# Kernel tuning notes

Measured on AMD Instinct MI355X. Metric: run time of the kernel, lower is better.

The kernel has to match this reference:

```python
import jax, jax.numpy as jnp
import numpy as np

NOOBJ_LAMBDA = 0.5
COORD_LAMBDA = 5.0


def _cxcywh_to_xyxy(b):
    cx, cy, w, h = b[..., 0], b[..., 1], b[..., 2], b[..., 3]
    return jnp.stack([cx - w / 2, cy - h / 2, cx + w / 2, cy + h / 2], axis=-1)


def _pairwise_iou(a, b):
    # a: [B, N, 4] xyxy (preds), b: [B, M, 4] xyxy (targets) -> [B, N, M]
    lt = jnp.maximum(a[:, :, None, :2], b[:, None, :, :2])
    rb = jnp.minimum(a[:, :, None, 2:], b[:, None, :, 2:])
    wh = jnp.clip(rb - lt, 0.0)
    inter = wh[..., 0] * wh[..., 1]
    area_a = (a[..., 2] - a[..., 0]) * (a[..., 3] - a[..., 1])
    area_b = (b[..., 2] - b[..., 0]) * (b[..., 3] - b[..., 1])
    union = area_a[:, :, None] + area_b[:, None, :] - inter
    return inter / jnp.where(union > 0, union, 1.0)


def setup_inputs() -> dict:
    key = jax.random.key(0)
    kp, kt, km = jax.random.split(key, 3)
    B = 8192
    # positive values so sqrt(w), sqrt(h) is well-defined (as the torch code assumes)
    pred = jax.random.uniform(kp, (B, 7, 7, 30), dtype=jnp.float32, minval=0.05, maxval=1.0)
    target = jax.random.uniform(kt, (B, 7, 7, 30), dtype=jnp.float32, minval=0.05, maxval=1.0)
    # target confidence channel (index 4) is the obj/noobj indicator: 0 or 1
    obj = (jax.random.uniform(km, (B, 7, 7)) < 0.2).astype(jnp.float32)
    target = target.at[..., 4].set(obj)
    return {"pred_tensor": pred, "target_tensor": target}


def reference(pred_tensor, target_tensor):
    B = pred_tensor.shape[0]
    pred = pred_tensor.reshape(B, 49, 30)
    target = target_tensor.reshape(B, 49, 30)

    conf_t = target[..., 4]            # [B,49]
    noobj = conf_t == 0                # [B,49]
    obj = conf_t > 0                   # [B,49]

    # --- no-object confidence loss (channels 4 and 9) ---
    d4 = pred[..., 4] - target[..., 4]
    d9 = pred[..., 9] - target[..., 9]
    noobj_loss = jnp.sum(jnp.where(noobj, d4 * d4 + d9 * d9, 0.0))

    # --- object cells: 2 boxes per cell, padded to all 49 cells with a mask ---
    pb = pred[..., :10].reshape(B, 98, 5)
    tb = target[..., :10].reshape(B, 98, 5)
    box_mask = jnp.repeat(obj, 2, axis=1)  # [B,98]

    p_xyxy = _cxcywh_to_xyxy(pb[..., :4])
    t_xyxy = _cxcywh_to_xyxy(tb[..., :4])
    iou = _pairwise_iou(p_xyxy, t_xyxy)  # [B,98,98]
    pair_mask = box_mask[:, :, None] & box_mask[:, None, :]
    iou = jnp.where(pair_mask, iou, 0.0)
    max_iou = jnp.max(iou, axis=1)       # max over pred boxes, per target box [B,98]
    cmask = (max_iou != 0) & box_mask    # [B,98]

    cm = cmask.astype(pred.dtype)
    # coord (cx,cy) loss
    dxy = pb[..., :2] - tb[..., :2]
    coord_loss_cxcy = jnp.sum(cm * jnp.sum(dxy * dxy, axis=-1))
    # coord (sqrt w, sqrt h) loss
    dwh = jnp.sqrt(pb[..., 2:4]) - jnp.sqrt(tb[..., 2:4])
    coord_loss_wh = jnp.sum(cm * jnp.sum(dwh * dwh, axis=-1))
    # object confidence loss
    dconf = pb[..., 4] - tb[..., 4]
    obj_loss = jnp.sum(cm * dconf * dconf)

    # --- class loss over object cells ---
    dcls = pred[..., 10:] - target[..., 10:]
    cls_loss = jnp.sum(obj.astype(pred.dtype) * jnp.sum(dcls * dcls, axis=-1))

    bsz = jnp.asarray(B, pred.dtype)
    batch_cls_loss = cls_loss / bsz
    batch_obj_loss = (obj_loss + noobj_loss * NOOBJ_LAMBDA) / bsz
    batch_coord_loss = (coord_loss_cxcy + coord_loss_wh) * COORD_LAMBDA / bsz
    batch_loss = batch_cls_loss + batch_obj_loss + batch_coord_loss
    return (batch_loss, batch_cls_loss, batch_obj_loss, batch_coord_loss)
```

## Files before the change

kernel.cpp:

```cpp
#include <hip/hip_runtime.h>

#define CH 30
#define CELLS 49
#define ROWF 1470
#define RPW 2
#define WPB 4
#define RPB 8
#define NPAIR 735
#define NQ4 735
#define ITS 12

__device__ __forceinline__ float waveReduce(float v) {
    #pragma unroll
    for (int o = 32; o > 0; o >>= 1) v += __shfl_xor(v, o, 64);
    return v;
}

__global__ __launch_bounds__(256) void yolo_main(const float* __restrict__ pred,
                                                 const float* __restrict__ targ,
                                                 float* __restrict__ ws, int B,
                                                 int NB) {
    const int w = threadIdx.x >> 6;
    const int lane = threadIdx.x & 63;
    const int r0 = (blockIdx.x * WPB + w) * RPW;

    __shared__ float4 boxS[WPB][2 * CELLS];
    __shared__ int clist[WPB][CELLS];
    __shared__ float sred[WPB][3];

    float cls = 0.f, objc = 0.f, coord = 0.f;

    if (r0 < B) {
        const int nrows = (B - r0) >= RPW ? RPW : 1;
        const float* P = pred + (size_t)r0 * ROWF;
        const float* T = targ + (size_t)r0 * ROWF;
        unsigned long long m[2] = {0ull, 0ull};

        if (nrows == 2) {
            const float4* P4 = (const float4*)P;
            const float4* T4 = (const float4*)T;

            const int cl = lane < CELLS ? lane : CELLS - 1;
            const float conf0 = T[cl * CH + 4];
            const float conf1 = T[ROWF + cl * CH + 4];

            float4 pv[ITS], tv[ITS];
            #pragma unroll
            for (int it = 0; it < ITS; ++it) {
                const int j = lane + it * 64;
                const int jc = j < NQ4 ? j : NQ4 - 1;
                pv[it] = P4[jc];
                tv[it] = T4[jc];
            }

            const bool o0 = (lane < CELLS) && (conf0 > 0.f);
            const bool o1 = (lane < CELLS) && (conf1 > 0.f);
            m[0] = __ballot(o0);
            m[1] = __ballot(o1);

            #pragma unroll
            for (int it = 0; it < ITS; ++it) {
                const int j = lane + it * 64;
                const bool valid = j < NQ4;
                #pragma unroll
                for (int k = 0; k < 2; ++k) {
                    const int q = 2 * j + k;
                    const int row = q >= NPAIR ? 1 : 0;
                    const int pr = q - row * NPAIR;
                    const int cell = (pr * 17477) >> 18;
                    const int ch0 = 2 * (pr - cell * 15);
                    const float wobj = (float)((m[row] >> cell) & 1ull);
                    const float px = k ? pv[it].z : pv[it].x;
                    const float py = k ? pv[it].w : pv[it].y;
                    const float tx = k ? tv[it].z : tv[it].x;
                    const float ty = k ? tv[it].w : tv[it].y;
                    const float dx = px - tx, dy = py - ty;
                    cls += (valid && ch0 >= 10) ? wobj * (dx * dx + dy * dy) : 0.f;
                    const float nn = (ch0 == 4 ? dx * dx : 0.f)
                                   + (ch0 == 8 ? dy * dy : 0.f);
                    objc += valid ? 0.5f * (1.f - wobj) * nn : 0.f;
                }
            }
        } else {
            const float2* P2 = (const float2*)P;
            const float2* T2 = (const float2*)T;
            const int cl = lane < CELLS ? lane : CELLS - 1;
            const float conf = T[cl * CH + 4];
            const bool isObj = (lane < CELLS) && (conf > 0.f);
            m[0] = __ballot(isObj);
            for (int j = lane; j < NPAIR; j += 64) {
                const float2 pq = P2[j], tq = T2[j];
                const int cell = (j * 17477) >> 18;
                const int ch0 = 2 * (j - cell * 15);
                const float wobj = (float)((m[0] >> cell) & 1ull);
                const float dx = pq.x - tq.x, dy = pq.y - tq.y;
                cls += (ch0 >= 10) ? wobj * (dx * dx + dy * dy) : 0.f;
                const float nn = (ch0 == 4 ? dx * dx : 0.f)
                               + (ch0 == 8 ? dy * dy : 0.f);
                objc += 0.5f * (1.f - wobj) * nn;
            }
        }

        for (int rr = 0; rr < nrows; ++rr) {
            const unsigned long long mask = m[rr];
            const int nBox = 2 * __popcll(mask);
            if (nBox == 0) continue;
            const float* Pr = P + rr * ROWF;
            const float* Tr = T + rr * ROWF;

            const bool isObj = (lane < CELLS) && ((mask >> lane) & 1ull);
            if (isObj) clist[w][__popcll(mask & ((1ull << lane) - 1ull))] = lane;

            for (int e = lane; e < nBox; e += 64) {
                const int c = clist[w][e >> 1];
                const float* pb = Pr + c * CH + (e & 1) * 5;
                const float cx = pb[0], cy = pb[1], bw = pb[2], bh = pb[3];
                boxS[w][e] = make_float4(cx - 0.5f * bw, cy - 0.5f * bh,
                                         cx + 0.5f * bw, cy + 0.5f * bh);
            }

            for (int e = lane; e < nBox; e += 64) {
                const int c = clist[w][e >> 1];
                const float* tb = Tr + c * CH + (e & 1) * 5;
                const float tcx = tb[0], tcy = tb[1], tw = tb[2], th = tb[3];
                const float tx1 = tcx - 0.5f * tw, ty1 = tcy - 0.5f * th;
                const float tx2 = tcx + 0.5f * tw, ty2 = tcy + 0.5f * th;
                const float ta = (tx2 - tx1) * (ty2 - ty1);
                float maxiou = 0.f;
                for (int i = 0; i < nBox; ++i) {
                    const float4 pb4 = boxS[w][i];
                    const float lx = fmaxf(pb4.x, tx1), ly = fmaxf(pb4.y, ty1);
                    const float rx = fminf(pb4.z, tx2), ry = fminf(pb4.w, ty2);
                    const float iw = fmaxf(rx - lx, 0.f), ih = fmaxf(ry - ly, 0.f);
                    const float inter = iw * ih;
                    const float pa = (pb4.z - pb4.x) * (pb4.w - pb4.y);
                    const float un = pa + ta - inter;
                    const float iou = inter / (un > 0.f ? un : 1.f);
                    maxiou = fmaxf(maxiou, iou);
                }
                if (maxiou != 0.f) {
                    const float* pb = Pr + c * CH + (e & 1) * 5;
                    const float dcx = pb[0] - tcx, dcy = pb[1] - tcy;
                    coord += dcx * dcx + dcy * dcy;
                    const float dw = sqrtf(pb[2]) - sqrtf(tw);
                    const float dh = sqrtf(pb[3]) - sqrtf(th);
                    coord += dw * dw + dh * dh;
                    const float dc = pb[4] - tb[4];
                    objc += dc * dc;
                }
            }
        }
    }

    cls = waveReduce(cls); objc = waveReduce(objc); coord = waveReduce(coord);
    if (lane == 0) { sred[w][0] = cls; sred[w][1] = objc; sred[w][2] = coord; }
    __syncthreads();
    if (threadIdx.x == 0) {
        float C = 0.f, O = 0.f, X = 0.f;
        #pragma unroll
        for (int k = 0; k < WPB; ++k) { C += sred[k][0]; O += sred[k][1]; X += sred[k][2]; }
        ws[blockIdx.x] = C;
        ws[NB + blockIdx.x] = O;
        ws[2 * NB + blockIdx.x] = X;
    }
}

__global__ __launch_bounds__(1024) void yolo_reduce(const float* __restrict__ ws,
                                                    float* __restrict__ out,
                                                    int NB, float invB) {
    const int tid = threadIdx.x;
    const int w = tid >> 6, lane = tid & 63;
    float c = 0.f, o = 0.f, x = 0.f;
    for (int i = tid; i < NB; i += 1024) {
        c += ws[i];
        o += ws[NB + i];
        x += ws[2 * NB + i];
    }
    c = waveReduce(c); o = waveReduce(o); x = waveReduce(x);
    __shared__ float sred[16][3];
    if (lane == 0) { sred[w][0] = c; sred[w][1] = o; sred[w][2] = x; }
    __syncthreads();
    if (tid == 0) {
        float C = 0.f, O = 0.f, X = 0.f;
        #pragma unroll
        for (int k = 0; k < 16; ++k) { C += sred[k][0]; O += sred[k][1]; X += sred[k][2]; }
        const float bcls = C * invB;
        const float bobj = O * invB;
        const float bcoord = X * 5.0f * invB;
        out[0] = bcls + bobj + bcoord;
        out[1] = bcls;
        out[2] = bobj;
        out[3] = bcoord;
    }
}

extern "C" void kernel_launch(void* const* d_in, const int* in_sizes, int n_in,
                              void* d_out, int out_size, void* d_ws, size_t ws_size,
                              hipStream_t stream) {
    const float* pred = (const float*)d_in[0];
    const float* targ = (const float*)d_in[1];
    float* ws = (float*)d_ws;
    float* out = (float*)d_out;
    const int B = in_sizes[0] / ROWF;
    const int NB = (B + RPB - 1) / RPB;

    yolo_main<<<NB, 256, 0, stream>>>(pred, targ, ws, B, NB);
    yolo_reduce<<<1, 1024, 0, stream>>>(ws, out, NB, 1.0f / (float)B);
}
```

Baseline: 125.7 us.

## Split each row pair across two waves with software-pipelined loads and occupancy hint

```diff
diff --git a/kernel.cpp b/kernel.cpp
--- a/kernel.cpp
+++ b/kernel.cpp
@@ -3,12 +3,11 @@
 #define CH 30
 #define CELLS 49
 #define ROWF 1470
-#define RPW 2
-#define WPB 4
-#define RPB 8
 #define NPAIR 735
 #define NQ4 735
-#define ITS 12
+#define WPB 4
+#define RPBLK 4
+#define HITS 6
 
 __device__ __forceinline__ float waveReduce(float v) {
     #pragma unroll
@@ -16,13 +15,14 @@
     return v;
 }
 
-__global__ __launch_bounds__(256) void yolo_main(const float* __restrict__ pred,
-                                                 const float* __restrict__ targ,
-                                                 float* __restrict__ ws, int B,
-                                                 int NB) {
+__global__ __launch_bounds__(256, 8) void yolo_main(const float* __restrict__ pred,
+                                                    const float* __restrict__ targ,
+                                                    float* __restrict__ ws, int B,
+                                                    int NB) {
     const int w = threadIdx.x >> 6;
     const int lane = threadIdx.x & 63;
-    const int r0 = (blockIdx.x * WPB + w) * RPW;
+    const int h = w & 1;
+    const int r0 = blockIdx.x * RPBLK + (w >> 1) * 2;
 
     __shared__ float4 boxS[WPB][2 * CELLS];
     __shared__ int clist[WPB][CELLS];
@@ -31,7 +31,7 @@
     float cls = 0.f, objc = 0.f, coord = 0.f;
 
     if (r0 < B) {
-        const int nrows = (B - r0) >= RPW ? RPW : 1;
+        const int nrows = (B - r0) >= 2 ? 2 : 1;
         const float* P = pred + (size_t)r0 * ROWF;
         const float* T = targ + (size_t)r0 * ROWF;
         unsigned long long m[2] = {0ull, 0ull};
@@ -44,109 +44,150 @@
             const float conf0 = T[cl * CH + 4];
             const float conf1 = T[ROWF + cl * CH + 4];
 
-            float4 pv[ITS], tv[ITS];
+            const int q0 = lane + h * 64;
+            const int q0c = q0 < NQ4 ? q0 : NQ4 - 1;
+            float4 pa = P4[q0c];
+            float4 ta = T4[q0c];
+
+            m[0] = __ballot((lane < CELLS) && (conf0 > 0.f));
+            m[1] = __ballot((lane < CELLS) && (conf1 > 0.f));
+
             #pragma unroll
-            for (int it = 0; it < ITS; ++it) {
-                const int j = lane + it * 64;
-                const int jc = j < NQ4 ? j : NQ4 - 1;
-                pv[it] = P4[jc];
-                tv[it] = T4[jc];
-            }
-
-            const bool o0 = (lane < CELLS) && (conf0 > 0.f);
-            const bool o1 = (lane < CELLS) && (conf1 > 0.f);
-            m[0] = __ballot(o0);
-            m[1] = __ballot(o1);
-
-            #pragma unroll
-            for (int it = 0; it < ITS; ++it) {
-                const int j = lane + it * 64;
-                const bool valid = j < NQ4;
+            for (int it = 0; it < HITS; ++it) {
+                float4 pb, tb;
+                if (it + 1 < HITS) {
+                    const int qn = lane + (2 * (it + 1) + h) * 64;
+                    const int qc = qn < NQ4 ? qn : NQ4 - 1;
+                    pb = P4[qc];
+                    tb = T4[qc];
+                }
+                const int qq = lane + (2 * it + h) * 64;
+                const bool valid = qq < NQ4;
                 #pragma unroll
                 for (int k = 0; k < 2; ++k) {
-                    const int q = 2 * j + k;
-                    const int row = q >= NPAIR ? 1 : 0;
-                    const int pr = q - row * NPAIR;
+                    const int p = 2 * qq + k;
+                    const int row = p >= NPAIR ? 1 : 0;
+                    const int pr = p - row * NPAIR;
                     const int cell = (pr * 17477) >> 18;
                     const int ch0 = 2 * (pr - cell * 15);
                     const float wobj = (float)((m[row] >> cell) & 1ull);
-                    const float px = k ? pv[it].z : pv[it].x;
-                    const float py = k ? pv[it].w : pv[it].y;
-                    const float tx = k ? tv[it].z : tv[it].x;
-                    const float ty = k ? tv[it].w : tv[it].y;
+                    const float px = k ? pa.z : pa.x;
+                    const float py = k ? pa.w : pa.y;
+                    const float tx = k ? ta.z : ta.x;
+                    const float ty = k ? ta.w : ta.y;
                     const float dx = px - tx, dy = py - ty;
                     cls += (valid && ch0 >= 10) ? wobj * (dx * dx + dy * dy) : 0.f;
                     const float nn = (ch0 == 4 ? dx * dx : 0.f)
                                    + (ch0 == 8 ? dy * dy : 0.f);
                     objc += valid ? 0.5f * (1.f - wobj) * nn : 0.f;
                 }
-            }
-        } else {
+                if (it + 1 < HITS) { pa = pb; ta = tb; }
+            }
+
+            const unsigned long long mask = m[h];
+            const int nBox = 2 * __popcll(mask);
+            if (nBox) {
+                const float* Pr = P + h * ROWF;
+                const float* Tr = T + h * ROWF;
+                const bool isObj = (lane < CELLS) && ((mask >> lane) & 1ull);
+                if (isObj) clist[w][__popcll(mask & ((1ull << lane) - 1ull))] = lane;
+
+                for (int e = lane; e < nBox; e += 64) {
+                    const int c = clist[w][e >> 1];
+                    const float* pb = Pr + c * CH + (e & 1) * 5;
+                    const float cx = pb[0], cy = pb[1], bw = pb[2], bh = pb[3];
+                    boxS[w][e] = make_float4(cx - 0.5f * bw, cy - 0.5f * bh,
+                                             cx + 0.5f * bw, cy + 0.5f * bh);
+                }
+
+                for (int e = lane; e < nBox; e += 64) {
+                    const int c = clist[w][e >> 1];
+                    const float* tb = Tr + c * CH + (e & 1) * 5;
+                    const float tcx = tb[0], tcy = tb[1], tw = tb[2], th = tb[3];
+                    const float tx1 = tcx - 0.5f * tw, ty1 = tcy - 0.5f * th;
+                    const float tx2 = tcx + 0.5f * tw, ty2 = tcy + 0.5f * th;
+                    const float ta2 = (tx2 - tx1) * (ty2 - ty1);
+                    float maxiou = 0.f;
+                    for (int i = 0; i < nBox; ++i) {
+                        const float4 pb4 = boxS[w][i];
+                        const float lx = fmaxf(pb4.x, tx1), ly = fmaxf(pb4.y, ty1);
+                        const float rx = fminf(pb4.z, tx2), ry = fminf(pb4.w, ty2);
+                        const float iw = fmaxf(rx - lx, 0.f), ih = fmaxf(ry - ly, 0.f);
+                        const float inter = iw * ih;
+                        const float pa2 = (pb4.z - pb4.x) * (pb4.w - pb4.y);
+                        const float un = pa2 + ta2 - inter;
+                        const float iou = inter / (un > 0.f ? un : 1.f);
+                        maxiou = fmaxf(maxiou, iou);
+                    }
+                    if (maxiou != 0.f) {
+                        const float* pb = Pr + c * CH + (e & 1) * 5;
+                        const float dcx = pb[0] - tcx, dcy = pb[1] - tcy;
+                        coord += dcx * dcx + dcy * dcy;
+                        const float dw = sqrtf(pb[2]) - sqrtf(tw);
+                        const float dh = sqrtf(pb[3]) - sqrtf(th);
+                        coord += dw * dw + dh * dh;
+                        const float dc = pb[4] - tb[4];
+                        objc += dc * dc;
+                    }
+                }
+            }
+        } else if (h == 0) {
             const float2* P2 = (const float2*)P;
             const float2* T2 = (const float2*)T;
             const int cl = lane < CELLS ? lane : CELLS - 1;
             const float conf = T[cl * CH + 4];
             const bool isObj = (lane < CELLS) && (conf > 0.f);
-            m[0] = __ballot(isObj);
+            const unsigned long long mask = __ballot(isObj);
             for (int j = lane; j < NPAIR; j += 64) {
                 const float2 pq = P2[j], tq = T2[j];
                 const int cell = (j * 17477) >> 18;
                 const int ch0 = 2 * (j - cell * 15);
-                const float wobj = (float)((m[0] >> cell) & 1ull);
+                const float wobj = (float)((mask >> cell) & 1ull);
                 const float dx = pq.x - tq.x, dy = pq.y - tq.y;
                 cls += (ch0 >= 10) ? wobj * (dx * dx + dy * dy) : 0.f;
                 const float nn = (ch0 == 4 ? dx * dx : 0.f)
                                + (ch0 == 8 ? dy * dy : 0.f);
                 objc += 0.5f * (1.f - wobj) * nn;
             }
-        }
-
-        for (int rr = 0; rr < nrows; ++rr) {
-            const unsigned long long mask = m[rr];
             const int nBox = 2 * __popcll(mask);
-            if (nBox == 0) continue;
-            const float* Pr = P + rr * ROWF;
-            const float* Tr = T + rr * ROWF;
-
-            const bool isObj = (lane < CELLS) && ((mask >> lane) & 1ull);
-            if (isObj) clist[w][__popcll(mask & ((1ull << lane) - 1ull))] = lane;
-
-            for (int e = lane; e < nBox; e += 64) {
-                const int c = clist[w][e >> 1];
-                const float* pb = Pr + c * CH + (e & 1) * 5;
-                const float cx = pb[0], cy = pb[1], bw = pb[2], bh = pb[3];
-                boxS[w][e] = make_float4(cx - 0.5f * bw, cy - 0.5f * bh,
-                                         cx + 0.5f * bw, cy + 0.5f * bh);
-            }
-
-            for (int e = lane; e < nBox; e += 64) {
-                const int c = clist[w][e >> 1];
-                const float* tb = Tr + c * CH + (e & 1) * 5;
-                const float tcx = tb[0], tcy = tb[1], tw = tb[2], th = tb[3];
-                const float tx1 = tcx - 0.5f * tw, ty1 = tcy - 0.5f * th;
-                const float tx2 = tcx + 0.5f * tw, ty2 = tcy + 0.5f * th;
-                const float ta = (tx2 - tx1) * (ty2 - ty1);
-                float maxiou = 0.f;
-                for (int i = 0; i < nBox; ++i) {
-                    const float4 pb4 = boxS[w][i];
-                    const float lx = fmaxf(pb4.x, tx1), ly = fmaxf(pb4.y, ty1);
-                    const float rx = fminf(pb4.z, tx2), ry = fminf(pb4.w, ty2);
-                    const float iw = fmaxf(rx - lx, 0.f), ih = fmaxf(ry - ly, 0.f);
-                    const float inter = iw * ih;
-                    const float pa = (pb4.z - pb4.x) * (pb4.w - pb4.y);
-                    const float un = pa + ta - inter;
-                    const float iou = inter / (un > 0.f ? un : 1.f);
-                    maxiou = fmaxf(maxiou, iou);
-                }
-                if (maxiou != 0.f) {
-                    const float* pb = Pr + c * CH + (e & 1) * 5;
-                    const float dcx = pb[0] - tcx, dcy = pb[1] - tcy;
-                    coord += dcx * dcx + dcy * dcy;
-                    const float dw = sqrtf(pb[2]) - sqrtf(tw);
-                    const float dh = sqrtf(pb[3]) - sqrtf(th);
-                    coord += dw * dw + dh * dh;
-                    const float dc = pb[4] - tb[4];
-                    objc += dc * dc;
+            if (nBox) {
+                if (isObj) clist[w][__popcll(mask & ((1ull << lane) - 1ull))] = lane;
+                for (int e = lane; e < nBox; e += 64) {
+                    const int c = clist[w][e >> 1];
+                    const float* pb = P + c * CH + (e & 1) * 5;
+                    const float cx = pb[0], cy = pb[1], bw = pb[2], bh = pb[3];
+                    boxS[w][e] = make_float4(cx - 0.5f * bw, cy - 0.5f * bh,
+                                             cx + 0.5f * bw, cy + 0.5f * bh);
+                }
+                for (int e = lane; e < nBox; e += 64) {
+                    const int c = clist[w][e >> 1];
+                    const float* tb = T + c * CH + (e & 1) * 5;
+                    const float tcx = tb[0], tcy = tb[1], tw = tb[2], th = tb[3];
+                    const float tx1 = tcx - 0.5f * tw, ty1 = tcy - 0.5f * th;
+                    const float tx2 = tcx + 0.5f * tw, ty2 = tcy + 0.5f * th;
+                    const float ta2 = (tx2 - tx1) * (ty2 - ty1);
+                    float maxiou = 0.f;
+                    for (int i = 0; i < nBox; ++i) {
+                        const float4 pb4 = boxS[w][i];
+                        const float lx = fmaxf(pb4.x, tx1), ly = fmaxf(pb4.y, ty1);
+                        const float rx = fminf(pb4.z, tx2), ry = fminf(pb4.w, ty2);
+                        const float iw = fmaxf(rx - lx, 0.f), ih = fmaxf(ry - ly, 0.f);
+                        const float inter = iw * ih;
+                        const float pa2 = (pb4.z - pb4.x) * (pb4.w - pb4.y);
+                        const float un = pa2 + ta2 - inter;
+                        const float iou = inter / (un > 0.f ? un : 1.f);
+                        maxiou = fmaxf(maxiou, iou);
+                    }
+                    if (maxiou != 0.f) {
+                        const float* pb = P + c * CH + (e & 1) * 5;
+                        const float dcx = pb[0] - tcx, dcy = pb[1] - tcy;
+                        coord += dcx * dcx + dcy * dcy;
+                        const float dw = sqrtf(pb[2]) - sqrtf(tw);
+                        const float dh = sqrtf(pb[3]) - sqrtf(th);
+                        coord += dw * dw + dh * dh;
+                        const float dc = pb[4] - tb[4];
+                        objc += dc * dc;
+                    }
                 }
             }
         }
@@ -202,7 +243,7 @@
     float* ws = (float*)d_ws;
     float* out = (float*)d_out;
     const int B = in_sizes[0] / ROWF;
-    const int NB = (B + RPB - 1) / RPB;
+    const int NB = (B + RPBLK - 1) / RPBLK;
 
     yolo_main<<<NB, 256, 0, stream>>>(pred, targ, ws, B, NB);
     yolo_reduce<<<1, 1024, 0, stream>>>(ws, out, NB, 1.0f / (float)B);
```

Result: faster. 120.6 us (-4.1%).
